# Performance work log

Measured on AMD Instinct MI355X. Metric: run time of the kernel, lower is better.

The kernel has to match this reference:

```python
import jax, jax.numpy as jnp
import numpy as np
import math

B, S, DIM = 2, 4096, 1024
H, HD = 16, 64            # n_heads, head_dim
BLK, TOPK = 512, 3        # moba_block_size, moba_topk
NEG_INF = -10000.0


def setup_inputs() -> dict:
    key = jax.random.key(0)
    ks = jax.random.split(key, 5)
    scale = 1.0 / math.sqrt(DIM)
    x = jax.random.normal(ks[0], (B, S, DIM), dtype=jnp.float32)
    wq = jax.random.normal(ks[1], (DIM, DIM), dtype=jnp.float32) * scale
    wk = jax.random.normal(ks[2], (DIM, DIM), dtype=jnp.float32) * scale
    wv = jax.random.normal(ks[3], (DIM, DIM), dtype=jnp.float32) * scale
    wo = jax.random.normal(ks[4], (DIM, DIM), dtype=jnp.float32) * scale
    # rotary tables over half of head_dim
    inv_freq = 1.0 / (10000.0 ** (jnp.arange(0, HD, 2, dtype=jnp.float32) / HD))
    ang = jnp.arange(S, dtype=jnp.float32)[:, None] * inv_freq[None, :]  # [S, HD//2]
    return {"x": x, "wq": wq, "wk": wk, "wv": wv, "wo": wo,
            "cos": jnp.cos(ang), "sin": jnp.sin(ang)}


def _rotate(t, cos, sin):
    # t: [B, H, S, HD]; rotate-half rotary embedding
    c = cos[None, None, :, :]
    s = sin[None, None, :, :]
    t1, t2 = jnp.split(t, 2, axis=-1)
    return jnp.concatenate([t1 * c - t2 * s, t1 * s + t2 * c], axis=-1)


def _moba_forward(x, wq, wk, wv, wo, cos, sin):
    bs, seq_len, dim = x.shape
    inv_sqrt_d = 1.0 / math.sqrt(HD)
    q = (x @ wq).reshape(bs, seq_len, H, HD).transpose(0, 2, 1, 3)  # [B,H,S,D]
    k = (x @ wk).reshape(bs, seq_len, H, HD).transpose(0, 2, 1, 3)
    v = (x @ wv).reshape(bs, seq_len, H, HD).transpose(0, 2, 1, 3)
    q = _rotate(q, cos, sin)
    k = _rotate(k, cos, sin)

    nb = seq_len // BLK  # num_blocks (S divisible by BLK -> pad_len = 0)
    k_blocks = k.reshape(bs, H, nb, BLK, HD)
    v_blocks = v.reshape(bs, H, nb, BLK, HD)

    # gating: q against block means, with block-causal mask
    block_repr = k_blocks.mean(axis=3)  # [B,H,nb,D]
    gating = jnp.einsum('bhsd,bhnd->bhsn', q, block_repr) * inv_sqrt_d
    q_block = jnp.arange(seq_len) // BLK
    future = q_block[:, None] < jnp.arange(nb)[None, :]  # [S, nb]
    gating = jnp.where(future[None, None], NEG_INF, gating)
    _, sel = jax.lax.top_k(gating, TOPK)  # [B,H,S,TOPK]

    # one chunk per block of queries; chunk uses indices of its middle query
    nc = seq_len // BLK
    mids = jnp.arange(nc) * BLK + BLK // 2
    chunk_sel = sel[:, :, mids, :]  # [B,H,nc,TOPK]

    idx = chunk_sel.reshape(bs, H, nc * TOPK)[..., None, None]  # [B,H,nc*k,1,1]
    k_sel = jnp.take_along_axis(k_blocks, idx, axis=2).reshape(bs, H, nc, TOPK * BLK, HD)
    v_sel = jnp.take_along_axis(v_blocks, idx, axis=2).reshape(bs, H, nc, TOPK * BLK, HD)

    q_ch = q.reshape(bs, H, nc, BLK, HD)
    scores = jnp.einsum('bhcqd,bhckd->bhcqk', q_ch, k_sel) * inv_sqrt_d
    probs = jax.nn.softmax(scores.astype(jnp.float32), axis=-1).astype(scores.dtype)
    out = jnp.einsum('bhcqk,bhckd->bhcqd', probs, v_sel)  # [B,H,nc,BLK,D]
    out = out.reshape(bs, H, seq_len, HD).transpose(0, 2, 1, 3).reshape(bs, seq_len, dim)
    return out @ wo


def reference(x, wq, wk, wv, wo, cos, sin):
    return _moba_forward(x, wq, wk, wv, wo, cos, sin)
```

## Files before the change

kernel.cpp:

```cpp
#include <hip/hip_runtime.h>

typedef short bf16x8 __attribute__((ext_vector_type(8)));
typedef float f32x4 __attribute__((ext_vector_type(4)));
typedef float f32x16 __attribute__((ext_vector_type(16)));

#define AS1 __attribute__((address_space(1)))
#define AS3 __attribute__((address_space(3)))
#define GLOAD16(g, l) __builtin_amdgcn_global_load_lds((const AS1 unsigned int*)(g), (AS3 unsigned int*)(l), 16, 0, 0)

#define B_   2
#define S_   4096
#define DIM_ 1024
#define H_   16
#define HD_  64
#define BLK_ 512
#define SCLQ 0.18033688011112042f

static __device__ __forceinline__ unsigned short f2bf(float x){
  unsigned int u = __builtin_bit_cast(unsigned int, x);
  u += 0x7fffu + ((u >> 16) & 1u);
  return (unsigned short)(u >> 16);
}

static __device__ __forceinline__ unsigned cvtpk(float lo, float hi){
  unsigned r;
  asm("v_cvt_pk_bf16_f32 %0, %1, %2" : "=v"(r) : "v"(lo), "v"(hi));
  return r;
}
static __device__ __forceinline__ void plswap(unsigned &a, unsigned &b){
  asm("v_permlane32_swap_b32 %0, %1" : "+v"(a), "+v"(b));
}
static __device__ __forceinline__ bf16x8 mkpa(unsigned a, unsigned b, unsigned c, unsigned d){
  int4 v = make_int4((int)a,(int)b,(int)c,(int)d);
  return __builtin_bit_cast(bf16x8, v);
}

__global__ __launch_bounds__(256) void k_convert_x(const float4* __restrict__ x, ushort4* __restrict__ xb){
  int i = blockIdx.x * 256 + threadIdx.x;
  float4 v = x[i];
  xb[i] = make_ushort4(f2bf(v.x), f2bf(v.y), f2bf(v.z), f2bf(v.w));
}

__global__ __launch_bounds__(256) void k_transpose_w(
    const float* __restrict__ w0, const float* __restrict__ w1,
    const float* __restrict__ w2, const float* __restrict__ w3,
    unsigned short* __restrict__ wqkvT, unsigned short* __restrict__ woT){
  __shared__ float tl[32][33];
  int z = blockIdx.z;
  const float* w = z==0 ? w0 : z==1 ? w1 : z==2 ? w2 : w3;
  unsigned short* t = (z==3) ? woT : (wqkvT + (size_t)z*1024*1024);
  int nb = blockIdx.x*32, kb = blockIdx.y*32;
  int tx = threadIdx.x & 31, ty = threadIdx.x >> 5;
  #pragma unroll
  for(int i=0;i<4;i++) tl[ty+8*i][tx] = w[(size_t)(kb+ty+8*i)*DIM_ + nb+tx];
  __syncthreads();
  #pragma unroll
  for(int i=0;i<4;i++) t[(size_t)(nb+ty+8*i)*DIM_ + kb+tx] = f2bf(tl[tx][ty+8*i]);
}

__global__ __launch_bounds__(256) void k_prepw(const float* __restrict__ cosT, const float* __restrict__ sinT,
                                               float* __restrict__ W){
  int idx = blockIdx.x*256 + threadIdx.x;
  int s = idx >> 6, j = idx & 63;
  W[idx] = (j < 32) ? cosT[s*32 + j] : sinT[s*32 + j - 32];
}

__global__ __launch_bounds__(256) void k_xp(const float* __restrict__ x, const float* __restrict__ W,
                                            float* __restrict__ Xp2){
  __shared__ float Xl[16*128];
  __shared__ float Wl[16*64];
  int bid = blockIdx.x;
  int dt = bid & 7, ss = (bid>>3)&1, n = (bid>>4)&7, b = bid>>7;
  int tid = threadIdx.x;
  int jt = tid & 15, dtl = tid >> 4;
  int dbase = dt*128;
  int s0 = n*512 + ss*256;
  f32x4 acc[8];
  #pragma unroll
  for(int i=0;i<8;i++) acc[i] = (f32x4){0.f,0.f,0.f,0.f};

  for(int ch=0; ch<16; ch++){
    int sb = s0 + ch*16;
    #pragma unroll
    for(int i=0;i<2;i++){
      int g = i*256 + tid;
      int row = g>>5, col = g&31;
      GLOAD16(x + ((size_t)b*S_ + sb + row)*DIM_ + dbase + col*4, (char*)Xl + g*16);
    }
    {
      int row = tid>>4, col = tid&15;
      GLOAD16(W + (size_t)(sb + row)*64 + col*4, (char*)Wl + tid*16);
    }
    __syncthreads();
    #pragma unroll
    for(int s=0;s<16;s++){
      f32x4 wv = *(const f32x4*)&Wl[s*64 + jt*4];
      f32x4 x0 = *(const f32x4*)&Xl[s*128 + dtl*8];
      f32x4 x1 = *(const f32x4*)&Xl[s*128 + dtl*8 + 4];
      #pragma unroll
      for(int dd=0;dd<4;dd++) acc[dd]   += wv * x0[dd];
      #pragma unroll
      for(int dd=0;dd<4;dd++) acc[dd+4] += wv * x1[dd];
    }
    __syncthreads();
  }
  size_t base = ((size_t)(ss*16 + b*8 + n))*1024;
  #pragma unroll
  for(int dd=0;dd<8;dd++){
    size_t row = base + dbase + dtl*8 + dd;
    *(f32x4*)&Xp2[row*64 + jt*4] = acc[dd];
  }
}

__global__ __launch_bounds__(256) void k_bsum(const float* __restrict__ Xp2, const float* __restrict__ wk,
                                              float* __restrict__ bsum){
  __shared__ float red[4][64];
  int bid = blockIdx.x;
  int h = bid & 15, n = (bid>>4)&7, b = bid>>7;
  int tid = threadIdx.x;
  int jj = tid & 63, dgrp = tid >> 6;
  int j = jj & 31;
  size_t r0 = ((size_t)(b*8 + n))*1024;
  size_t r1 = ((size_t)(16 + b*8 + n))*1024;
  float acc = 0.0f;
  for(int i=0;i<256;i++){
    int d = dgrp*256 + i;
    float xc = Xp2[(r0 + d)*64 + j]      + Xp2[(r1 + d)*64 + j];
    float xs = Xp2[(r0 + d)*64 + 32 + j] + Xp2[(r1 + d)*64 + 32 + j];
    float u = wk[(size_t)d*1024 + h*64 + j];
    float v = wk[(size_t)d*1024 + h*64 + 32 + j];
    acc += (jj < 32) ? (xc*u - xs*v) : (xs*u + xc*v);
  }
  red[dgrp][jj] = acc;
  __syncthreads();
  if(tid < 64){
    float s = red[0][tid] + red[1][tid] + red[2][tid] + red[3][tid];
    bsum[(((size_t)(b*16+h))*8 + n)*64 + tid] = s;
  }
}

__global__ __launch_bounds__(256) void k_qmid(const float* __restrict__ x, const float* __restrict__ wq,
                                              float* __restrict__ qpart){
  __shared__ float xr[128];
  int bid = blockIdx.x;
  int ks  = blockIdx.y;
  int b = bid >> 3, c = bid & 7;
  int mid = c*BLK_ + BLK_/2;
  int tid = threadIdx.x;
  if(tid < 128) xr[tid] = x[((size_t)b*S_ + mid)*DIM_ + ks*128 + tid];
  __syncthreads();
  float acc[4] = {0,0,0,0};
  for(int k=0;k<128;k++){
    float xv = xr[k];
    #pragma unroll
    for(int i=0;i<4;i++) acc[i] += xv * wq[(size_t)(ks*128+k)*1024 + i*256 + tid];
  }
  #pragma unroll
  for(int i=0;i<4;i++) qpart[((size_t)ks*16 + bid)*1024 + i*256 + tid] = acc[i];
}

__global__ __launch_bounds__(256) void k_qred(const float* __restrict__ qpart, float* __restrict__ qmid){
  int idx = blockIdx.x*256 + threadIdx.x;
  float s = 0.0f;
  #pragma unroll
  for(int ks=0;ks<8;ks++) s += qpart[(size_t)ks*16384 + idx];
  qmid[idx] = s;
}

__global__ __launch_bounds__(256) void k_sel(const float* __restrict__ qmid, const float* __restrict__ bsum,
                                             const float* __restrict__ cosT, const float* __restrict__ sinT,
                                             int* __restrict__ sel){
  int bid = blockIdx.x;
  int b = bid >> 3, c = bid & 7;
  int mid = c*BLK_ + BLK_/2;
  int tid = threadIdx.x;
  int hg = tid >> 4, ln = tid & 15;
  const float* qm = qmid + (size_t)bid*1024 + hg*64;
  float rv[4];
  #pragma unroll
  for(int i=0;i<4;i++){
    int jj = ln*4 + i; int j = jj & 31;
    float q1 = qm[j], q2 = qm[32+j];
    float c0 = cosT[(size_t)mid*32 + j], s0 = sinT[(size_t)mid*32 + j];
    rv[i] = (jj < 32) ? (q1*c0 - q2*s0) : (q1*s0 + q2*c0);
  }
  float g[8];
  #pragma unroll
  for(int n=0;n<8;n++){
    const float* bs = bsum + (((size_t)(b*16+hg))*8 + n)*64 + ln*4;
    float p = rv[0]*bs[0] + rv[1]*bs[1] + rv[2]*bs[2] + rv[3]*bs[3];
    p += __shfl_xor(p,1); p += __shfl_xor(p,2); p += __shfl_xor(p,4); p += __shfl_xor(p,8);
    g[n] = p * (1.0f/512.0f) * 0.125f;
  }
  if(ln == 0){
    for(int n=c+1;n<8;n++) g[n] = -10000.0f;
    int base = ((b*16+hg)*8 + c)*3;
    #pragma unroll
    for(int t=0;t<3;t++){
      int bi = 0; float bv = g[0];
      for(int n=1;n<8;n++) if(g[n] > bv){ bv = g[n]; bi = n; }
      sel[base + t] = bi;
      g[bi] = -3.4e38f;
    }
  }
}

template<int MODE>
__global__ __launch_bounds__(256) void k_gemm(const unsigned short* __restrict__ A,
                                              const unsigned short* __restrict__ Bt,
                                              unsigned short* __restrict__ dq, unsigned short* __restrict__ dk,
                                              unsigned short* __restrict__ dv, float* __restrict__ dstf,
                                              const float* __restrict__ cosT, const float* __restrict__ sinT,
                                              int M, int N, int K){
  __shared__ unsigned short lA[2][128*32];
  __shared__ unsigned short lB[2][128*32];
  int bm = blockIdx.y*128, bn = blockIdx.x*128;
  int tid = threadIdx.x, wave = tid>>6, lane = tid&63;
  int wr = wave>>1, wc = wave&1;
  int l15 = lane&15, lh = lane>>4;
  f32x4 acc[4][4];
  f32x4 zero = {0.f,0.f,0.f,0.f};
  #pragma unroll
  for(int m=0;m<4;m++)
    #pragma unroll
    for(int n=0;n<4;n++) acc[m][n] = zero;

  auto STAGE = [&](int bsel, int k0){
    #pragma unroll
    for(int i=0;i<2;i++){
      int g = i*256 + wave*64 + lane;
      int row = g>>2, c8 = (g&3)*8;
      GLOAD16(A  + (size_t)(bm+row)*K + k0 + c8, (char*)lA[bsel] + (i*256 + wave*64)*16);
      GLOAD16(Bt + (size_t)(bn+row)*K + k0 + c8, (char*)lB[bsel] + (i*256 + wave*64)*16);
    }
  };

  STAGE(0, 0);
  __syncthreads();
  int cur = 0;
  for(int k0=0;k0<K;k0+=32){
    if(k0+32 < K) STAGE(cur^1, k0+32);
    bf16x8 af[4], bfr[4];
    #pragma unroll
    for(int m=0;m<4;m++) af[m] = *(const bf16x8*)&lA[cur][(wr*64 + m*16 + l15)*32 + lh*8];
    #pragma unroll
    for(int n=0;n<4;n++) bfr[n] = *(const bf16x8*)&lB[cur][(wc*64 + n*16 + l15)*32 + lh*8];
    __builtin_amdgcn_s_setprio(1);
    #pragma unroll
    for(int m=0;m<4;m++)
      #pragma unroll
      for(int n=0;n<4;n++)
        acc[m][n] = __builtin_amdgcn_mfma_f32_16x16x32_bf16(af[m], bfr[n], acc[m][n], 0, 0, 0);
    __builtin_amdgcn_s_setprio(0);
    __syncthreads();
    cur ^= 1;
  }

  if(MODE == 2){
    #pragma unroll
    for(int m=0;m<4;m++){
      int row0 = bm + wr*64 + m*16 + lh*4;
      #pragma unroll
      for(int n=0;n<4;n++){
        int col = bn + wc*64 + n*16 + l15;
        #pragma unroll
        for(int r=0;r<4;r++) dstf[(size_t)(row0+r)*N + col] = acc[m][n][r];
      }
    }
  } else {
    int sec = bn >> 10;
    int nloc = (bn & 1023) + wc*64;
    if(sec == 2){
      #pragma unroll
      for(int m=0;m<4;m++){
        int s0 = bm + wr*64 + m*16 + lh*4;
        int bb = s0 >> 12, sl = s0 & 4095;
        #pragma unroll
        for(int n=0;n<4;n++){
          int d = nloc + n*16 + l15;
          ushort4 pk = make_ushort4(f2bf(acc[m][n][0]), f2bf(acc[m][n][1]),
                                    f2bf(acc[m][n][2]), f2bf(acc[m][n][3]));
          *(ushort4*)&dv[((size_t)(bb*1024 + d))*4096 + sl] = pk;
        }
      }
    } else {
      unsigned short* dst = (sec == 0) ? dq : dk;
      float scl = (sec == 0) ? SCLQ : 1.0f;
      int h = nloc >> 6;
      #pragma unroll
      for(int m=0;m<4;m++){
        int row0 = bm + wr*64 + m*16 + lh*4;
        #pragma unroll
        for(int n=0;n<2;n++){
          int f = n*16 + l15;
          #pragma unroll
          for(int r=0;r<4;r++){
            int row = row0 + r;
            int bb = row >> 12, s = row & 4095;
            float c0 = cosT[(size_t)s*32 + f]*scl, s0 = sinT[(size_t)s*32 + f]*scl;
            float a1 = acc[m][n][r], a2 = acc[m][n+2][r];
            size_t base = ((size_t)(bb*16 + h)*4096 + s)*64;
            dst[base + f]      = f2bf(a1*c0 - a2*s0);
            dst[base + 32 + f] = f2bf(a1*s0 + a2*c0);
          }
        }
      }
    }
  }
}

__global__ __launch_bounds__(256, 4) void k_attn(const unsigned short* __restrict__ q,
                                                 const unsigned short* __restrict__ kb,
                                                 const unsigned short* __restrict__ vt,
                                                 const int* __restrict__ sel,
                                                 unsigned short* __restrict__ attnb){
  __shared__ unsigned short lK[2][64*64];
  __shared__ unsigned short lV[2][64*64];
  int cbh = blockIdx.x, qt = blockIdx.y;
  int bh = cbh >> 3, c = cbh & 7;
  int b = bh >> 4, h = bh & 15;
  int tid = threadIdx.x, w = tid>>6, lane = tid&63;
  int ql = lane&31, hi = lane>>5;
  int q0 = c*BLK_ + qt*128 + w*32;

  const int* selp = sel + (bh*8 + c)*3;
  int sb0 = selp[0], sb1 = selp[1], sb2 = selp[2];

  int r0 = tid>>3, sl = (tid&7) ^ (r0&7);
  const unsigned short* kbase = kb + ((size_t)bh*S_ + r0)*64 + (size_t)sl*8;
  const unsigned short* vbase = vt + ((size_t)(b*1024 + h*64 + r0))*S_ + (size_t)sl*8;

  bf16x8 qf[4];
  #pragma unroll
  for(int kk=0;kk<4;kk++)
    qf[kk] = *(const bf16x8*)(q + ((size_t)bh*S_ + q0 + ql)*64 + kk*16 + hi*8);

  f32x16 o[2], o2;
  f32x16 zero16 = {0,0,0,0,0,0,0,0,0,0,0,0,0,0,0,0};
  o[0] = zero16; o[1] = zero16; o2 = zero16;
  short one_bf = (short)0x3F80;
  bf16x8 ones = {one_bf,one_bf,one_bf,one_bf,one_bf,one_bf,one_bf,one_bf};

  auto STAGE = [&](int bsel, int t){
    int seg = t>>3;
    int blk = seg==0 ? sb0 : (seg==1 ? sb1 : sb2);
    int soff = blk*BLK_ + (t&7)*64;
    #pragma unroll
    for(int i=0;i<2;i++){
      GLOAD16(kbase + (size_t)(soff + i*32)*64, (char*)lK[bsel] + (i*256 + w*64)*16);
      GLOAD16(vbase + (size_t)i*32*S_ + soff,   (char*)lV[bsel] + (i*256 + w*64)*16);
    }
  };

  STAGE(0, 0);
  __syncthreads();
  int cur = 0;

  for(int t=0;t<24;t++){
    if(t+1 < 24) STAGE(cur^1, t+1);

    f32x16 sc[2];
    sc[0] = zero16; sc[1] = zero16;
    __builtin_amdgcn_s_setprio(1);
    #pragma unroll
    for(int g=0;g<2;g++){
      int key = g*32 + ql;
      #pragma unroll
      for(int kk=0;kk<4;kk++){
        bf16x8 kf = *(const bf16x8*)((const char*)lK[cur] + key*128 + ((kk*32 + hi*16) ^ ((ql&7)<<4)));
        sc[g] = __builtin_amdgcn_mfma_f32_32x32x16_bf16(kf, qf[kk], sc[g], 0, 0, 0);
      }
    }
    __builtin_amdgcn_s_setprio(0);

    #pragma unroll
    for(int r=0;r<16;r++){
      sc[0][r] = exp2f(sc[0][r]);
      sc[1][r] = exp2f(sc[1][r]);
    }

    __builtin_amdgcn_s_setprio(1);
    #pragma unroll
    for(int g=0;g<2;g++){
      unsigned u0 = cvtpk(sc[g][0],  sc[g][1]);
      unsigned u1 = cvtpk(sc[g][4],  sc[g][5]);
      plswap(u0, u1);
      unsigned u2 = cvtpk(sc[g][2],  sc[g][3]);
      unsigned u3 = cvtpk(sc[g][6],  sc[g][7]);
      plswap(u2, u3);
      unsigned u4 = cvtpk(sc[g][8],  sc[g][9]);
      unsigned u5 = cvtpk(sc[g][12], sc[g][13]);
      plswap(u4, u5);
      unsigned u6 = cvtpk(sc[g][10], sc[g][11]);
      unsigned u7 = cvtpk(sc[g][14], sc[g][15]);
      plswap(u6, u7);
      bf16x8 pa0 = mkpa(u0,u2,u1,u3);
      bf16x8 pa1 = mkpa(u4,u6,u5,u7);
      #pragma unroll
      for(int dh=0;dh<2;dh++){
        int d = dh*32 + ql;
        bf16x8 v0 = *(const bf16x8*)((const char*)lV[cur] + d*128 + ((g*64 + hi*16) ^ ((d&7)<<4)));
        o[dh] = __builtin_amdgcn_mfma_f32_32x32x16_bf16(pa0, v0, o[dh], 0, 0, 0);
        bf16x8 v1 = *(const bf16x8*)((const char*)lV[cur] + d*128 + ((g*64 + 32 + hi*16) ^ ((d&7)<<4)));
        o[dh] = __builtin_amdgcn_mfma_f32_32x32x16_bf16(pa1, v1, o[dh], 0, 0, 0);
      }
      o2 = __builtin_amdgcn_mfma_f32_32x32x16_bf16(pa0, ones, o2, 0, 0, 0);
      o2 = __builtin_amdgcn_mfma_f32_32x32x16_bf16(pa1, ones, o2, 0, 0, 0);
    }
    __builtin_amdgcn_s_setprio(0);

    __syncthreads();
    cur ^= 1;
  }

  #pragma unroll
  for(int r=0;r<16;r++){
    float inv = 1.0f / o2[r];
    int cr = (r&3) + 8*(r>>2) + 4*hi;
    int s = q0 + cr;
    size_t base = ((size_t)(b*S_ + s))*1024 + h*64;
    attnb[base + ql]      = f2bf(o[0][r]*inv);
    attnb[base + 32 + ql] = f2bf(o[1][r]*inv);
  }
}

extern "C" void kernel_launch(void* const* d_in, const int* in_sizes, int n_in,
                              void* d_out, int out_size, void* d_ws, size_t ws_size,
                              hipStream_t stream){
  const float* x    = (const float*)d_in[0];
  const float* wq   = (const float*)d_in[1];
  const float* wk   = (const float*)d_in[2];
  const float* wv   = (const float*)d_in[3];
  const float* wo   = (const float*)d_in[4];
  const float* cosT = (const float*)d_in[5];
  const float* sinT = (const float*)d_in[6];

  char* p = (char*)d_ws;
  unsigned short* xbf   = (unsigned short*)p; p += (size_t)8192*1024*2;
  unsigned short* wqkvT = (unsigned short*)p; p += (size_t)3072*1024*2;
  unsigned short* woT   = (unsigned short*)p; p += (size_t)1024*1024*2;
  unsigned short* qb  = (unsigned short*)p; p += (size_t)8192*1024*2;
  unsigned short* kbf = (unsigned short*)p; p += (size_t)8192*1024*2;
  unsigned short* vtb = (unsigned short*)p; p += (size_t)8192*1024*2;
  float* Wsel = (float*)p; p += (size_t)4096*64*4;
  float* Xp2  = (float*)p; p += (size_t)2*16*1024*64*4;
  float* bsum = (float*)p; p += (size_t)2*16*8*64*4;
  float* qmid = (float*)p; p += (size_t)16*1024*4;
  int*   sel  = (int*)p;   p += (size_t)2*16*8*3*4;
  unsigned short* attnb = xbf;
  float* qpart = Wsel;
  if((size_t)(p - (char*)d_ws) > ws_size) return;

  k_convert_x<<<8192, 256, 0, stream>>>((const float4*)x, (ushort4*)xbf);
  k_transpose_w<<<dim3(32,32,4), 256, 0, stream>>>(wq,wk,wv,wo, wqkvT, woT);
  k_prepw<<<1024, 256, 0, stream>>>(cosT, sinT, Wsel);
  k_xp<<<256, 256, 0, stream>>>(x, Wsel, Xp2);
  k_bsum<<<256, 256, 0, stream>>>(Xp2, wk, bsum);
  k_qmid<<<dim3(16,8), 256, 0, stream>>>(x, wq, qpart);
  k_qred<<<64, 256, 0, stream>>>(qpart, qmid);
  k_sel<<<16, 256, 0, stream>>>(qmid, bsum, cosT, sinT, sel);
  k_gemm<0><<<dim3(24,64), 256, 0, stream>>>(xbf, wqkvT, qb, kbf, vtb, nullptr, cosT, sinT, 8192, 3072, 1024);
  k_attn<<<dim3(256,4), 256, 0, stream>>>(qb, kbf, vtb, sel, attnb);
  k_gemm<2><<<dim3(8,64), 256, 0, stream>>>(attnb, woT, nullptr, nullptr, nullptr, (float*)d_out, nullptr, nullptr, 8192, 1024, 1024);
}
```

Before: 282.7 us.

## Retile GEMM to 256x128x64 with swizzled LDS and deeper async prefetch

Replaces the 128x128 GEMM tile (256 threads, K-step 32) with a 256x128 tile using 512 threads and a K-step of 64. LDS rows are XOR-swizzled to avoid bank conflicts. The loop now prefetches two stages ahead, using explicit vmcnt waits and raw barriers in place of __syncthreads. The aim is more data reuse per tile, fewer LDS conflicts and better overlap of global loads with MFMA, at the cost of more LDS per block and hand-managed wait counts that must match the number of loads issued.

Result: faster. 273.2 us (-3.3%).

```diff
diff --git a/kernel.cpp b/kernel.cpp
--- a/kernel.cpp
+++ b/kernel.cpp
@@ -206,17 +206,17 @@
 }
 
 template<int MODE>
-__global__ __launch_bounds__(256) void k_gemm(const unsigned short* __restrict__ A,
-                                              const unsigned short* __restrict__ Bt,
-                                              unsigned short* __restrict__ dq, unsigned short* __restrict__ dk,
-                                              unsigned short* __restrict__ dv, float* __restrict__ dstf,
-                                              const float* __restrict__ cosT, const float* __restrict__ sinT,
-                                              int M, int N, int K){
-  __shared__ unsigned short lA[2][128*32];
-  __shared__ unsigned short lB[2][128*32];
-  int bm = blockIdx.y*128, bn = blockIdx.x*128;
-  int tid = threadIdx.x, wave = tid>>6, lane = tid&63;
-  int wr = wave>>1, wc = wave&1;
+__global__ __launch_bounds__(512, 2) void k_gemmq(const unsigned short* __restrict__ A,
+                                                  const unsigned short* __restrict__ Bt,
+                                                  unsigned short* __restrict__ dq, unsigned short* __restrict__ dk,
+                                                  unsigned short* __restrict__ dv, float* __restrict__ dstf,
+                                                  const float* __restrict__ cosT, const float* __restrict__ sinT,
+                                                  int M, int N, int K){
+  __shared__ unsigned short lA[2][256*64];
+  __shared__ unsigned short lB[2][128*64];
+  int bm = blockIdx.y*256, bn = blockIdx.x*128;
+  int tid = threadIdx.x, w = tid>>6, lane = tid&63;
+  int wr = w>>1, wc = w&1;
   int l15 = lane&15, lh = lane>>4;
   f32x4 acc[4][4];
   f32x4 zero = {0.f,0.f,0.f,0.f};
@@ -227,32 +227,53 @@
 
   auto STAGE = [&](int bsel, int k0){
     #pragma unroll
+    for(int i=0;i<4;i++){
+      int g = i*512 + tid;
+      int row = g>>3, slot = (g&7)^(row&7);
+      GLOAD16(A + (size_t)(bm+row)*K + k0 + slot*8, (char*)lA[bsel] + g*16);
+    }
+    #pragma unroll
     for(int i=0;i<2;i++){
-      int g = i*256 + wave*64 + lane;
-      int row = g>>2, c8 = (g&3)*8;
-      GLOAD16(A  + (size_t)(bm+row)*K + k0 + c8, (char*)lA[bsel] + (i*256 + wave*64)*16);
-      GLOAD16(Bt + (size_t)(bn+row)*K + k0 + c8, (char*)lB[bsel] + (i*256 + wave*64)*16);
+      int g = i*512 + tid;
+      int row = g>>3, slot = (g&7)^(row&7);
+      GLOAD16(Bt + (size_t)(bn+row)*K + k0 + slot*8, (char*)lB[bsel] + g*16);
     }
   };
 
+  int NT = K >> 6;
   STAGE(0, 0);
-  __syncthreads();
+  STAGE(1, 64);
   int cur = 0;
-  for(int k0=0;k0<K;k0+=32){
-    if(k0+32 < K) STAGE(cur^1, k0+32);
-    bf16x8 af[4], bfr[4];
-    #pragma unroll
-    for(int m=0;m<4;m++) af[m] = *(const bf16x8*)&lA[cur][(wr*64 + m*16 + l15)*32 + lh*8];
-    #pragma unroll
-    for(int n=0;n<4;n++) bfr[n] = *(const bf16x8*)&lB[cur][(wc*64 + n*16 + l15)*32 + lh*8];
-    __builtin_amdgcn_s_setprio(1);
-    #pragma unroll
-    for(int m=0;m<4;m++)
-      #pragma unroll
-      for(int n=0;n<4;n++)
-        acc[m][n] = __builtin_amdgcn_mfma_f32_16x16x32_bf16(af[m], bfr[n], acc[m][n], 0, 0, 0);
-    __builtin_amdgcn_s_setprio(0);
-    __syncthreads();
+
+  for(int t=0;t<NT;t++){
+    if(t < NT-1) asm volatile("s_waitcnt vmcnt(6)" ::: "memory");
+    else         asm volatile("s_waitcnt vmcnt(0)" ::: "memory");
+    asm volatile("s_barrier" ::: "memory");
+
+    #pragma unroll
+    for(int kk=0;kk<2;kk++){
+      bf16x8 af[4], bfr[4];
+      #pragma unroll
+      for(int m=0;m<4;m++){
+        int r = wr*64 + m*16 + l15;
+        af[m] = *(const bf16x8*)((const char*)lA[cur] + r*128 + (((kk*4+lh)^(r&7))*16));
+      }
+      #pragma unroll
+      for(int n=0;n<4;n++){
+        int r = wc*64 + n*16 + l15;
+        bfr[n] = *(const bf16x8*)((const char*)lB[cur] + r*128 + (((kk*4+lh)^(r&7))*16));
+      }
+      __builtin_amdgcn_s_setprio(1);
+      #pragma unroll
+      for(int m=0;m<4;m++)
+        #pragma unroll
+        for(int n=0;n<4;n++)
+          acc[m][n] = __builtin_amdgcn_mfma_f32_16x16x32_bf16(af[m], bfr[n], acc[m][n], 0, 0, 0);
+      __builtin_amdgcn_s_setprio(0);
+    }
+
+    asm volatile("s_barrier" ::: "memory");
+    if(t+2 < NT) STAGE(cur, (t+2)*64);
     cur ^= 1;
   }
 
@@ -459,7 +480,7 @@
   k_qmid<<<dim3(16,8), 256, 0, stream>>>(x, wq, qpart);
   k_qred<<<64, 256, 0, stream>>>(qpart, qmid);
   k_sel<<<16, 256, 0, stream>>>(qmid, bsum, cosT, sinT, sel);
-  k_gemm<0><<<dim3(24,64), 256, 0, stream>>>(xbf, wqkvT, qb, kbf, vtb, nullptr, cosT, sinT, 8192, 3072, 1024);
+  k_gemmq<0><<<dim3(24,32), 512, 0, stream>>>(xbf, wqkvT, qb, kbf, vtb, nullptr, cosT, sinT, 8192, 3072, 1024);
   k_attn<<<dim3(256,4), 256, 0, stream>>>(qb, kbf, vtb, sel, attnb);
-  k_gemm<2><<<dim3(8,64), 256, 0, stream>>>(attnb, woT, nullptr, nullptr, nullptr, (float*)d_out, nullptr, nullptr, 8192, 1024, 1024);
-}
+  k_gemmq<2><<<dim3(8,32), 512, 0, stream>>>(attnb, woT, nullptr, nullptr, nullptr, (float*)d_out, nullptr, nullptr, 8192, 1024, 1024);
+}
```
